# Kernel optimization log

Hardware: AMD Instinct MI355X
Metric: run time of the kernel (lower is better)

Reference implementation:

```python
import jax, jax.numpy as jnp
import numpy as np

N_NODES = 100000
N_EDGES = 1600000
IN_DIM = 256
HID = 128
OUT_DIM = 2
N_LAYERS = 4
BN_EPS = 1e-5


def setup_inputs() -> dict:
    key = jax.random.key(0)
    ks = jax.random.split(key, 10)
    s_in = 1.0 / np.sqrt(IN_DIM)
    s_h = 1.0 / np.sqrt(HID)
    return {
        "x": jax.random.normal(ks[0], (N_NODES, IN_DIM), dtype=jnp.float32),
        "edge_index": jax.random.randint(ks[1], (2, N_EDGES), 0, N_NODES, dtype=jnp.int32),
        "W_in": jax.random.normal(ks[2], (IN_DIM, HID), dtype=jnp.float32) * s_in,
        "b_in": jnp.zeros((HID,), dtype=jnp.float32),
        # SAGEConv per-layer weights: lin_l (aggregated neighbors), lin_r (self/root)
        "W_l": jax.random.normal(ks[3], (N_LAYERS, HID, HID), dtype=jnp.float32) * s_h,
        "b_l": jnp.zeros((N_LAYERS, HID), dtype=jnp.float32),
        "W_r": jax.random.normal(ks[4], (N_LAYERS, HID, HID), dtype=jnp.float32) * s_h,
        "b_r": jnp.zeros((N_LAYERS, HID), dtype=jnp.float32),
        # BatchNorm (eval mode) params/buffers
        "bn_gamma": jnp.ones((N_LAYERS, HID), dtype=jnp.float32),
        "bn_beta": jnp.zeros((N_LAYERS, HID), dtype=jnp.float32),
        "bn_mean": jax.random.normal(ks[5], (N_LAYERS, HID), dtype=jnp.float32) * 0.01,
        "bn_var": jnp.ones((N_LAYERS, HID), dtype=jnp.float32),
        "W_cls": jax.random.normal(ks[6], (HID, OUT_DIM), dtype=jnp.float32) * s_h,
        "b_cls": jnp.zeros((OUT_DIM,), dtype=jnp.float32),
    }


def _sage_mean(h, src, dst, n):
    # gather source-node features along edges, scatter-mean at targets
    msg = h[src]  # [E, HID] -- the large irregular gather
    agg = jax.ops.segment_sum(msg, dst, num_segments=n)  # [N, HID]
    cnt = jax.ops.segment_sum(jnp.ones((src.shape[0],), h.dtype), dst, num_segments=n)
    return agg / jnp.maximum(cnt, 1.0)[:, None]


def reference(x, edge_index, W_in, b_in, W_l, b_l, W_r, b_r,
              bn_gamma, bn_beta, bn_mean, bn_var, W_cls, b_cls):
    n = x.shape[0]
    src, dst = edge_index[0], edge_index[1]
    h = jax.nn.relu(x @ W_in + b_in)  # dropout is identity at eval
    for i in range(N_LAYERS):
        h_in = h
        mean = _sage_mean(h, src, dst, n)
        h = mean @ W_l[i] + b_l[i] + h @ W_r[i] + b_r[i]
        # BatchNorm1d in eval mode (running stats)
        h = bn_gamma[i] * (h - bn_mean[i]) * jax.lax.rsqrt(bn_var[i] + BN_EPS) + bn_beta[i]
        h = jax.nn.relu(h)
        h = h + h_in
    return jax.nn.log_softmax(h @ W_cls + b_cls, axis=1)
```

## Files before the change

### kernel.cpp

```cpp
#include <hip/hip_runtime.h>

typedef unsigned int uint;
typedef unsigned short ushort;
typedef __attribute__((ext_vector_type(8))) short short8v;
typedef __attribute__((ext_vector_type(4))) float f32x4;

#define IN_DIM 256
#define HID 128
#define BN_EPS 1e-5f

__device__ __forceinline__ float bf2f(ushort u) { return __uint_as_float(((uint)u) << 16); }
__device__ __forceinline__ ushort f2bf(float f) {
    uint u = __float_as_uint(f);
    return (ushort)((u + 0x7fffu + ((u >> 16) & 1u)) >> 16);
}
__device__ __forceinline__ uint cvt_pk_bf16(float a, float b) {
    uint r;
    asm("v_cvt_pk_bf16_f32 %0, %1, %2" : "=v"(r) : "v"(a), "v"(b));
    return r;
}
__device__ __forceinline__ void gload_lds16(const void* g, void* l) {
    __builtin_amdgcn_global_load_lds(
        (const __attribute__((address_space(1))) uint*)g,
        (__attribute__((address_space(3))) uint*)l, 16, 0, 0);
}


__global__ __launch_bounds__(256) void hist_kernel(const int* __restrict__ ei,
                                                   int* __restrict__ histG,
                                                   int E, int chunk) {
    __shared__ int hcnt[256];
    int t = threadIdx.x;
    hcnt[t] = 0;
    __syncthreads();
    int e0 = blockIdx.x * chunk;
    int e1 = min(E, e0 + chunk);
    for (int e = e0 + t; e < e1; e += 256)
        atomicAdd(&hcnt[__builtin_nontemporal_load(ei + E + e) >> 9], 1);
    __syncthreads();
    histG[blockIdx.x * 256 + t] = hcnt[t];
}

__global__ __launch_bounds__(256) void basescan_kernel(const int* __restrict__ histG,
                                                       int* __restrict__ baseG,
                                                       int* __restrict__ bucketStart,
                                                       int nchunk, int nbuck, int E) {
    __shared__ int sA[256], sB[256];
    int t = threadIdx.x;
    int tot = 0;
    for (int c = 0; c < nchunk; c++) tot += histG[c * 256 + t];
    sA[t] = tot;
    __syncthreads();
    int* src = sA; int* dst = sB;
    for (int off = 1; off < 256; off <<= 1) {
        int v = src[t];
        if (t >= off) v += src[t - off];
        dst[t] = v;
        __syncthreads();
        int* tmp = src; src = dst; dst = tmp;
    }
    int excl = src[t] - tot;
    if (t < nbuck) bucketStart[t] = excl;
    if (t == 0) bucketStart[nbuck] = E;
    int running = excl;
    for (int c = 0; c < nchunk; c++) {
        baseG[c * 256 + t] = running;
        running += histG[c * 256 + t];
    }
}

__global__ __launch_bounds__(256) void partition_kernel(const int* __restrict__ ei,
                                                        const int* __restrict__ baseG,
                                                        uint2* __restrict__ ebuck,
                                                        int E, int chunk) {
    __shared__ int cur[256];
    int t = threadIdx.x;
    cur[t] = baseG[blockIdx.x * 256 + t];
    __syncthreads();
    int e0 = blockIdx.x * chunk;
    int e1 = min(E, e0 + chunk);
    for (int e = e0 + t; e < e1; e += 256) {
        int d = __builtin_nontemporal_load(ei + E + e);
        int s = __builtin_nontemporal_load(ei + e);
        int pos = atomicAdd(&cur[d >> 9], 1);
        ebuck[pos] = make_uint2((uint)s, (uint)d);
    }
}

__global__ __launch_bounds__(256) void bucket_build(const uint2* __restrict__ ebuck,
                                                    const int* __restrict__ bucketStart,
                                                    int* __restrict__ row_ptr,
                                                    int* __restrict__ esrc,
                                                    int n, int nbuck) {
    __shared__ int deg[512];
    __shared__ int sA[512], sB[512];
    __shared__ int cur[512];
    __shared__ int img[16384];
    int b = blockIdx.x;
    int t = threadIdx.x;
    int lo = b << 9;
    int hi = min(n, lo + 512);
    int nn = hi - lo;
    int eStart = bucketStart[b];
    int eEnd = bucketStart[b + 1];
    int cnt = eEnd - eStart;
    for (int i = t; i < 512; i += 256) deg[i] = 0;
    __syncthreads();
    for (int e = eStart + t; e < eEnd; e += 256) {
        uint2 p = ebuck[e];
        atomicAdd(&deg[(int)p.y - lo], 1);
    }
    __syncthreads();
    for (int i = t; i < 512; i += 256) sA[i] = deg[i];
    __syncthreads();
    int* src = sA; int* dst = sB;
    for (int off = 1; off < 512; off <<= 1) {
        for (int i = t; i < 512; i += 256) {
            int v = src[i];
            if (i >= off) v += src[i - off];
            dst[i] = v;
        }
        __syncthreads();
        int* tmp = src; src = dst; dst = tmp;
    }
    for (int i = t; i < 512; i += 256) cur[i] = src[i] - deg[i];
    __syncthreads();
    for (int i = t; i < nn; i += 256) row_ptr[lo + i] = eStart + cur[i];
    if (b == nbuck - 1 && t == 0) row_ptr[n] = eEnd;
    __syncthreads();
    if (cnt <= 16384) {
        for (int e = eStart + t; e < eEnd; e += 256) {
            uint2 p = ebuck[e];
            int pos = atomicAdd(&cur[(int)p.y - lo], 1);
            img[pos] = (int)p.x;
        }
        __syncthreads();
        for (int i = t; i < cnt; i += 256) esrc[eStart + i] = img[i];
    } else {
        for (int e = eStart + t; e < eEnd; e += 256) {
            uint2 p = ebuck[e];
            int pos = atomicAdd(&cur[(int)p.y - lo], 1);
            esrc[eStart + pos] = (int)p.x;
        }
    }
}


__global__ __launch_bounds__(256) void pack_win(const float* __restrict__ W, ushort* __restrict__ Wt) {
    int idx = blockIdx.x * 256 + threadIdx.x;
    int k = idx >> 7, c = idx & 127;
    Wt[c * IN_DIM + k] = f2bf(W[idx]);
}

__global__ __launch_bounds__(256) void pack_wcat(const float* __restrict__ Wl,
                                                 const float* __restrict__ Wr,
                                                 ushort* __restrict__ Wt) {
    int idx = blockIdx.x * 256 + threadIdx.x;
    int layer = idx >> 15;
    int rem = idx & 32767;
    int k = rem >> 7, c = rem & 127;
    float v = (k < HID) ? Wl[layer * HID * HID + k * HID + c]
                        : Wr[layer * HID * HID + (k - HID) * HID + c];
    Wt[layer * (HID * 256) + c * 256 + k] = f2bf(v);
}


__global__ __launch_bounds__(256) void sage_mean_bf16(const ushort* __restrict__ h,
                                                      const int* __restrict__ row_ptr,
                                                      const int* __restrict__ esrc,
                                                      ushort* __restrict__ meanb, int n) {
    int node = blockIdx.x * 4 + (threadIdx.x >> 6);
    if (node >= n) return;
    int lane = threadIdx.x & 63;
    int start = row_ptr[node];
    int end = row_ptr[node + 1];
    float ax = 0.f, ay = 0.f;
    int j = start;
    for (; j + 15 < end; j += 16) {
        uint v[16];
        #pragma unroll
        for (int q = 0; q < 16; q++)
            v[q] = *(const uint*)(h + (size_t)esrc[j + q] * HID + lane * 2);
        #pragma unroll
        for (int q = 0; q < 16; q++) {
            ax += bf2f((ushort)(v[q] & 0xffffu));
            ay += bf2f((ushort)(v[q] >> 16));
        }
    }
    for (; j + 7 < end; j += 8) {
        uint v[8];
        #pragma unroll
        for (int q = 0; q < 8; q++)
            v[q] = *(const uint*)(h + (size_t)esrc[j + q] * HID + lane * 2);
        #pragma unroll
        for (int q = 0; q < 8; q++) {
            ax += bf2f((ushort)(v[q] & 0xffffu));
            ay += bf2f((ushort)(v[q] >> 16));
        }
    }
    for (; j < end; ++j) {
        uint v0 = *(const uint*)(h + (size_t)esrc[j] * HID + lane * 2);
        ax += bf2f((ushort)(v0 & 0xffffu));
        ay += bf2f((ushort)(v0 >> 16));
    }
    int deg = end - start;
    float inv = 1.0f / (float)(deg > 1 ? deg : 1);
    uint o = (uint)f2bf(ax * inv) | (((uint)f2bf(ay * inv)) << 16);
    *(uint*)(meanb + (size_t)node * HID + lane * 2) = o;
}


__global__ __launch_bounds__(256) void input_gemm_mfma(const float* __restrict__ x,
                                                       const ushort* __restrict__ Wt,
                                                       const float* __restrict__ b,
                                                       ushort* __restrict__ hout, int n) {
    __shared__ float Axs[32 * IN_DIM];
    int t = threadIdx.x;
    int l = t & 63;
    int wv = t >> 6;
    int colbase = wv * 32;
    int lr = l & 15;
    int grp = l >> 4;
    int ko = grp * 8;

    short8v Bf[8][2];
    #pragma unroll
    for (int ks = 0; ks < 8; ks++) {
        #pragma unroll
        for (int nt = 0; nt < 2; nt++) {
            int c = colbase + nt * 16 + lr;
            Bf[ks][nt] = *(const short8v*)(Wt + (size_t)c * IN_DIM + ks * 32 + ko);
        }
    }
    float bias0 = b[colbase + lr];
    float bias1 = b[colbase + 16 + lr];

    int ntiles = (n + 31) >> 5;
    for (int tile = blockIdx.x; tile < ntiles; tile += gridDim.x) {
        int row0 = tile * 32;
        __syncthreads();
        {
            const char* xb = (const char*)(x + (size_t)row0 * IN_DIM);
            char* lb = (char*)Axs;
            #pragma unroll
            for (int i = 0; i < 8; i++) {
                int off = i * 4096 + t * 16;
                int src = off ^ (((off >> 10) & 7) << 4);
                gload_lds16(xb + src, lb + i * 4096 + wv * 1024);
            }
        }
        __syncthreads();
        f32x4 acc00 = {0.f,0.f,0.f,0.f}, acc01 = {0.f,0.f,0.f,0.f};
        f32x4 acc10 = {0.f,0.f,0.f,0.f}, acc11 = {0.f,0.f,0.f,0.f};
        #pragma unroll
        for (int m = 0; m < 2; m++) {
            int r = m * 16 + lr;
            int rswz = (r & 7) << 4;
            const char* rowp = (const char*)Axs + r * 1024;
            short8v Af[8];
            #pragma unroll
            for (int ks = 0; ks < 8; ks++) {
                int kb = (ko + ks * 32) * 4;
                float4 p = *(const float4*)(rowp + (kb ^ rswz));
                float4 q = *(const float4*)(rowp + ((kb + 16) ^ rswz));
                union { uint4 u; short8v s; } cv;
                cv.u.x = cvt_pk_bf16(p.x, p.y);
                cv.u.y = cvt_pk_bf16(p.z, p.w);
                cv.u.z = cvt_pk_bf16(q.x, q.y);
                cv.u.w = cvt_pk_bf16(q.z, q.w);
                Af[ks] = cv.s;
            }
            if (m == 0) {
                #pragma unroll
                for (int ks = 0; ks < 8; ks++) {
                    acc00 = __builtin_amdgcn_mfma_f32_16x16x32_bf16(Af[ks], Bf[ks][0], acc00, 0, 0, 0);
                    acc01 = __builtin_amdgcn_mfma_f32_16x16x32_bf16(Af[ks], Bf[ks][1], acc01, 0, 0, 0);
                }
            } else {
                #pragma unroll
                for (int ks = 0; ks < 8; ks++) {
                    acc10 = __builtin_amdgcn_mfma_f32_16x16x32_bf16(Af[ks], Bf[ks][0], acc10, 0, 0, 0);
                    acc11 = __builtin_amdgcn_mfma_f32_16x16x32_bf16(Af[ks], Bf[ks][1], acc11, 0, 0, 0);
                }
            }
        }
        #pragma unroll
        for (int m = 0; m < 2; m++) {
            int rbase = row0 + m * 16 + grp * 4;
            f32x4 a0 = m == 0 ? acc00 : acc10;
            f32x4 a1 = m == 0 ? acc01 : acc11;
            #pragma unroll
            for (int r = 0; r < 4; r++) {
                int rowd = rbase + r;
                if (rowd < n) {
                    float z0 = a0[r] + bias0; z0 = z0 > 0.f ? z0 : 0.f;
                    float z1 = a1[r] + bias1; z1 = z1 > 0.f ? z1 : 0.f;
                    hout[(size_t)rowd * HID + colbase + lr] = f2bf(z0);
                    hout[(size_t)rowd * HID + colbase + 16 + lr] = f2bf(z1);
                }
            }
        }
    }
}


__global__ __launch_bounds__(256) void sage_layer_mfma(const ushort* __restrict__ h,
                                                       const ushort* __restrict__ mh,
                                                       ushort* __restrict__ hout,
                                                       const ushort* __restrict__ Wt,
                                                       const float* __restrict__ bl,
                                                       const float* __restrict__ br,
                                                       const float* __restrict__ gamma,
                                                       const float* __restrict__ beta,
                                                       const float* __restrict__ bmean,
                                                       const float* __restrict__ bvar,
                                                       int n) {
    __shared__ ushort Ams[64 * HID];
    __shared__ ushort Ahs[64 * HID];
    int t = threadIdx.x;
    int l = t & 63;
    int wv = t >> 6;
    int colbase = wv * 32;
    int lr = l & 15;
    int grp = l >> 4;
    int ko = grp * 8;

    short8v Bf[8][2];
    #pragma unroll
    for (int ks = 0; ks < 8; ks++) {
        #pragma unroll
        for (int nt = 0; nt < 2; nt++) {
            int c = colbase + nt * 16 + lr;
            Bf[ks][nt] = *(const short8v*)(Wt + (size_t)c * 256 + ks * 32 + ko);
        }
    }
    int c0 = colbase + lr;
    int c1 = c0 + 16;
    float scale0 = gamma[c0] * rsqrtf(bvar[c0] + BN_EPS);
    float scale1 = gamma[c1] * rsqrtf(bvar[c1] + BN_EPS);
    float shift0 = beta[c0] + (bl[c0] + br[c0] - bmean[c0]) * scale0;
    float shift1 = beta[c1] + (bl[c1] + br[c1] - bmean[c1]) * scale1;

    int ntiles = (n + 63) >> 6;
    for (int tile = blockIdx.x; tile < ntiles; tile += gridDim.x) {
        int row0 = tile * 64;
        __syncthreads();
        {
            const char* mb = (const char*)(mh + (size_t)row0 * HID);
            const char* hb = (const char*)(h + (size_t)row0 * HID);
            char* lm = (char*)Ams;
            char* lh = (char*)Ahs;
            #pragma unroll
            for (int i = 0; i < 4; i++) {
                int off = i * 4096 + t * 16;
                int src = off ^ (((off >> 8) & 7) << 4);
                gload_lds16(mb + src, lm + i * 4096 + wv * 1024);
                gload_lds16(hb + src, lh + i * 4096 + wv * 1024);
            }
        }
        __syncthreads();
        #pragma unroll
        for (int m = 0; m < 4; m++) {
            int r = m * 16 + lr;
            int rswz = (r & 7) << 4;
            const char* mrow = (const char*)Ams + r * 256;
            const char* hrow = (const char*)Ahs + r * 256;
            short8v Af[8];
            #pragma unroll
            for (int ks = 0; ks < 4; ks++) {
                int kb = (ko + ks * 32) * 2;
                Af[ks] = *(const short8v*)(mrow + (kb ^ rswz));
            }
            #pragma unroll
            for (int ks = 4; ks < 8; ks++) {
                int kb = (ko + (ks - 4) * 32) * 2;
                Af[ks] = *(const short8v*)(hrow + (kb ^ rswz));
            }
            f32x4 acc0 = {0.f,0.f,0.f,0.f};
            f32x4 acc1 = {0.f,0.f,0.f,0.f};
            #pragma unroll
            for (int ks = 0; ks < 8; ks++) {
                acc0 = __builtin_amdgcn_mfma_f32_16x16x32_bf16(Af[ks], Bf[ks][0], acc0, 0, 0, 0);
                acc1 = __builtin_amdgcn_mfma_f32_16x16x32_bf16(Af[ks], Bf[ks][1], acc1, 0, 0, 0);
            }
            int rbase = m * 16 + grp * 4;
            #pragma unroll
            for (int r2 = 0; r2 < 4; r2++) {
                int rloc = rbase + r2;
                int rowd = row0 + rloc;
                if (rowd < n) {
                    int rs = (rloc & 7) << 4;
                    float res0 = bf2f(*(const ushort*)((const char*)Ahs + rloc * 256 + ((c0 * 2) ^ rs)));
                    float res1 = bf2f(*(const ushort*)((const char*)Ahs + rloc * 256 + ((c1 * 2) ^ rs)));
                    float z0 = acc0[r2] * scale0 + shift0; z0 = z0 > 0.f ? z0 : 0.f;
                    float z1 = acc1[r2] * scale1 + shift1; z1 = z1 > 0.f ? z1 : 0.f;
                    hout[(size_t)rowd * HID + c0] = f2bf(z0 + res0);
                    hout[(size_t)rowd * HID + c1] = f2bf(z1 + res1);
                }
            }
        }
    }
}


__global__ __launch_bounds__(256) void classifier_bf16(const ushort* __restrict__ h,
                                                       const float* __restrict__ Wc,
                                                       const float* __restrict__ bc,
                                                       float* __restrict__ outp, int n) {
    __shared__ float Wcs[HID * 2];
    int t = threadIdx.x;
    if (t < 64) *(float4*)&Wcs[t * 4] = *(const float4*)&Wc[t * 4];
    __syncthreads();
    int rowInBlk = t >> 4;
    int sub = t & 15;
    int row = blockIdx.x * 16 + rowInBlk;
    float l0 = 0.f, l1 = 0.f;
    if (row < n) {
        const ushort* hr = h + (size_t)row * HID + sub * 8;
        uint4 v = *(const uint4*)hr;
        float e0 = bf2f((ushort)(v.x & 0xffffu)), e1 = bf2f((ushort)(v.x >> 16));
        float e2 = bf2f((ushort)(v.y & 0xffffu)), e3 = bf2f((ushort)(v.y >> 16));
        float e4 = bf2f((ushort)(v.z & 0xffffu)), e5 = bf2f((ushort)(v.z >> 16));
        float e6 = bf2f((ushort)(v.w & 0xffffu)), e7 = bf2f((ushort)(v.w >> 16));
        int k0 = sub * 8;
        l0 += e0 * Wcs[(k0 + 0) * 2] + e1 * Wcs[(k0 + 1) * 2] + e2 * Wcs[(k0 + 2) * 2] + e3 * Wcs[(k0 + 3) * 2];
        l0 += e4 * Wcs[(k0 + 4) * 2] + e5 * Wcs[(k0 + 5) * 2] + e6 * Wcs[(k0 + 6) * 2] + e7 * Wcs[(k0 + 7) * 2];
        l1 += e0 * Wcs[(k0 + 0) * 2 + 1] + e1 * Wcs[(k0 + 1) * 2 + 1] + e2 * Wcs[(k0 + 2) * 2 + 1] + e3 * Wcs[(k0 + 3) * 2 + 1];
        l1 += e4 * Wcs[(k0 + 4) * 2 + 1] + e5 * Wcs[(k0 + 5) * 2 + 1] + e6 * Wcs[(k0 + 6) * 2 + 1] + e7 * Wcs[(k0 + 7) * 2 + 1];
    }
    #pragma unroll
    for (int off = 1; off < 16; off <<= 1) {
        l0 += __shfl_xor(l0, off);
        l1 += __shfl_xor(l1, off);
    }
    if (sub == 0 && row < n) {
        l0 += bc[0];
        l1 += bc[1];
        float m = fmaxf(l0, l1);
        float lse = m + logf(expf(l0 - m) + expf(l1 - m));
        outp[(size_t)row * 2 + 0] = l0 - lse;
        outp[(size_t)row * 2 + 1] = l1 - lse;
    }
}


extern "C" void kernel_launch(void* const* d_in, const int* in_sizes, int n_in,
                              void* d_out, int out_size, void* d_ws, size_t ws_size,
                              hipStream_t stream) {
    const float* x     = (const float*)d_in[0];
    const int*   ei    = (const int*)d_in[1];
    const float* W_in  = (const float*)d_in[2];
    const float* b_in  = (const float*)d_in[3];
    const float* W_l   = (const float*)d_in[4];
    const float* b_l   = (const float*)d_in[5];
    const float* W_r   = (const float*)d_in[6];
    const float* b_r   = (const float*)d_in[7];
    const float* bn_g  = (const float*)d_in[8];
    const float* bn_b  = (const float*)d_in[9];
    const float* bn_m  = (const float*)d_in[10];
    const float* bn_v  = (const float*)d_in[11];
    const float* W_cls = (const float*)d_in[12];
    const float* b_cls = (const float*)d_in[13];
    float* outp = (float*)d_out;

    const int N = in_sizes[0] / IN_DIM;
    const int E = in_sizes[1] / 2;

    char* w = (char*)d_ws;
    const size_t HB = (size_t)N * HID * sizeof(ushort);
    ushort* hA     = (ushort*)(w);
    ushort* hB     = (ushort*)(w + HB);
    ushort* meanb  = (ushort*)(w + 2 * HB);
    ushort* Wt_in  = (ushort*)(w + 3 * HB);
    ushort* WcatT  = (ushort*)(w + 3 * HB + 65536);
    size_t off = 3 * HB + 65536 + 262144;
    int* row_ptr = (int*)(w + off);  off += ((size_t)(N + 1) * 4 + 255) & ~(size_t)255;
    int* esrc    = (int*)(w + off);  off += (size_t)E * 4;
    uint2* ebuck = (uint2*)(w + off); off += (size_t)E * 8;
    int* histG   = (int*)(w + off);  off += 256 * 256 * 4;
    int* baseG   = (int*)(w + off);  off += 256 * 256 * 4;
    int* bucketStart = (int*)(w + off); off += 4096;

    const int nbuck = (N + 511) >> 9;
    const int nchunk = 256;
    const int chunk = (E + nchunk - 1) / nchunk;

    pack_win<<<128, 256, 0, stream>>>(W_in, Wt_in);
    pack_wcat<<<512, 256, 0, stream>>>(W_l, W_r, WcatT);

    hist_kernel<<<nchunk, 256, 0, stream>>>(ei, histG, E, chunk);
    basescan_kernel<<<1, 256, 0, stream>>>(histG, baseG, bucketStart, nchunk, nbuck, E);
    partition_kernel<<<nchunk, 256, 0, stream>>>(ei, baseG, ebuck, E, chunk);
    bucket_build<<<nbuck, 256, 0, stream>>>(ebuck, bucketStart, row_ptr, esrc, N, nbuck);

    input_gemm_mfma<<<(N + 31) / 32, 256, 0, stream>>>(x, Wt_in, b_in, hA, N);

    ushort* hcur = hA;
    ushort* hoth = hB;
    for (int i = 0; i < 4; i++) {
        sage_mean_bf16<<<(N + 3) / 4, 256, 0, stream>>>(hcur, row_ptr, esrc, meanb, N);
        sage_layer_mfma<<<(N + 63) / 64, 256, 0, stream>>>(hcur, meanb, hoth,
                                                  WcatT + (size_t)i * HID * 256,
                                                  b_l + i * HID, b_r + i * HID,
                                                  bn_g + i * HID, bn_b + i * HID,
                                                  bn_m + i * HID, bn_v + i * HID, N);
        ushort* tmp = hcur; hcur = hoth; hoth = tmp;
    }

    classifier_bf16<<<(N + 15) / 16, 256, 0, stream>>>(hcur, W_cls, b_cls, outp, N);
}
```

Before: 529.5 us.

## Fuse neighbor mean aggregation into SAGE layer GEMM kernel via LDS

The separate mean-aggregation kernel is removed. Each wave of the layer kernel now gathers and averages neighbor features for 16 rows of its 64-row tile, writing the bf16 means straight into swizzled LDS before the MFMA step. This drops the write and re-read of the mean buffer and one launch per layer. The cost is that the irregular gather now runs in a kernel with large LDS and register use, so it may get less occupancy and latency hiding than the standalone kernel had, and the gather and GEMM phases are serialized within each block.

```diff
diff --git a/kernel.cpp b/kernel.cpp
--- a/kernel.cpp
+++ b/kernel.cpp
@@ -165,51 +165,6 @@
 }
 
 
-__global__ __launch_bounds__(256) void sage_mean_bf16(const ushort* __restrict__ h,
-                                                      const int* __restrict__ row_ptr,
-                                                      const int* __restrict__ esrc,
-                                                      ushort* __restrict__ meanb, int n) {
-    int node = blockIdx.x * 4 + (threadIdx.x >> 6);
-    if (node >= n) return;
-    int lane = threadIdx.x & 63;
-    int start = row_ptr[node];
-    int end = row_ptr[node + 1];
-    float ax = 0.f, ay = 0.f;
-    int j = start;
-    for (; j + 15 < end; j += 16) {
-        uint v[16];
-        #pragma unroll
-        for (int q = 0; q < 16; q++)
-            v[q] = *(const uint*)(h + (size_t)esrc[j + q] * HID + lane * 2);
-        #pragma unroll
-        for (int q = 0; q < 16; q++) {
-            ax += bf2f((ushort)(v[q] & 0xffffu));
-            ay += bf2f((ushort)(v[q] >> 16));
-        }
-    }
-    for (; j + 7 < end; j += 8) {
-        uint v[8];
-        #pragma unroll
-        for (int q = 0; q < 8; q++)
-            v[q] = *(const uint*)(h + (size_t)esrc[j + q] * HID + lane * 2);
-        #pragma unroll
-        for (int q = 0; q < 8; q++) {
-            ax += bf2f((ushort)(v[q] & 0xffffu));
-            ay += bf2f((ushort)(v[q] >> 16));
-        }
-    }
-    for (; j < end; ++j) {
-        uint v0 = *(const uint*)(h + (size_t)esrc[j] * HID + lane * 2);
-        ax += bf2f((ushort)(v0 & 0xffffu));
-        ay += bf2f((ushort)(v0 >> 16));
-    }
-    int deg = end - start;
-    float inv = 1.0f / (float)(deg > 1 ? deg : 1);
-    uint o = (uint)f2bf(ax * inv) | (((uint)f2bf(ay * inv)) << 16);
-    *(uint*)(meanb + (size_t)node * HID + lane * 2) = o;
-}
-
-
 __global__ __launch_bounds__(256) void input_gemm_mfma(const float* __restrict__ x,
                                                        const ushort* __restrict__ Wt,
                                                        const float* __restrict__ b,
@@ -304,17 +259,18 @@
 }
 
 
-__global__ __launch_bounds__(256) void sage_layer_mfma(const ushort* __restrict__ h,
-                                                       const ushort* __restrict__ mh,
-                                                       ushort* __restrict__ hout,
-                                                       const ushort* __restrict__ Wt,
-                                                       const float* __restrict__ bl,
-                                                       const float* __restrict__ br,
-                                                       const float* __restrict__ gamma,
-                                                       const float* __restrict__ beta,
-                                                       const float* __restrict__ bmean,
-                                                       const float* __restrict__ bvar,
-                                                       int n) {
+__global__ __launch_bounds__(256) void sage_fused(const ushort* __restrict__ h,
+                                                  ushort* __restrict__ hout,
+                                                  const int* __restrict__ row_ptr,
+                                                  const int* __restrict__ esrc,
+                                                  const ushort* __restrict__ Wt,
+                                                  const float* __restrict__ bl,
+                                                  const float* __restrict__ br,
+                                                  const float* __restrict__ gamma,
+                                                  const float* __restrict__ beta,
+                                                  const float* __restrict__ bmean,
+                                                  const float* __restrict__ bvar,
+                                                  int n) {
     __shared__ ushort Ams[64 * HID];
     __shared__ ushort Ahs[64 * HID];
     int t = threadIdx.x;
@@ -346,17 +302,56 @@
         int row0 = tile * 64;
         __syncthreads();
         {
-            const char* mb = (const char*)(mh + (size_t)row0 * HID);
             const char* hb = (const char*)(h + (size_t)row0 * HID);
-            char* lm = (char*)Ams;
             char* lh = (char*)Ahs;
             #pragma unroll
             for (int i = 0; i < 4; i++) {
                 int off = i * 4096 + t * 16;
                 int src = off ^ (((off >> 8) & 7) << 4);
-                gload_lds16(mb + src, lm + i * 4096 + wv * 1024);
                 gload_lds16(hb + src, lh + i * 4096 + wv * 1024);
             }
+        }
+        for (int i = 0; i < 16; i++) {
+            int r = wv * 16 + i;
+            int node = row0 + r;
+            float ax = 0.f, ay = 0.f;
+            if (node < n) {
+                int start = row_ptr[node];
+                int end = row_ptr[node + 1];
+                int j = start;
+                for (; j + 15 < end; j += 16) {
+                    uint v[16];
+                    #pragma unroll
+                    for (int q = 0; q < 16; q++)
+                        v[q] = *(const uint*)(h + (size_t)esrc[j + q] * HID + l * 2);
+                    #pragma unroll
+                    for (int q = 0; q < 16; q++) {
+                        ax += bf2f((ushort)(v[q] & 0xffffu));
+                        ay += bf2f((ushort)(v[q] >> 16));
+                    }
+                }
+                for (; j + 7 < end; j += 8) {
+                    uint v[8];
+                    #pragma unroll
+                    for (int q = 0; q < 8; q++)
+                        v[q] = *(const uint*)(h + (size_t)esrc[j + q] * HID + l * 2);
+                    #pragma unroll
+                    for (int q = 0; q < 8; q++) {
+                        ax += bf2f((ushort)(v[q] & 0xffffu));
+                        ay += bf2f((ushort)(v[q] >> 16));
+                    }
+                }
+                for (; j < end; ++j) {
+                    uint v0 = *(const uint*)(h + (size_t)esrc[j] * HID + l * 2);
+                    ax += bf2f((ushort)(v0 & 0xffffu));
+                    ay += bf2f((ushort)(v0 >> 16));
+                }
+                int deg = end - start;
+                float inv = 1.0f / (float)(deg > 1 ? deg : 1);
+                ax *= inv; ay *= inv;
+            }
+            uint o = (uint)f2bf(ax) | (((uint)f2bf(ay)) << 16);
+            *(uint*)((char*)Ams + r * 256 + ((l * 4) ^ ((r & 7) << 4))) = o;
         }
         __syncthreads();
         #pragma unroll
@@ -480,6 +475,7 @@
     int* histG   = (int*)(w + off);  off += 256 * 256 * 4;
     int* baseG   = (int*)(w + off);  off += 256 * 256 * 4;
     int* bucketStart = (int*)(w + off); off += 4096;
+    (void)meanb;
 
     const int nbuck = (N + 511) >> 9;
     const int nchunk = 256;
@@ -498,12 +494,11 @@
     ushort* hcur = hA;
     ushort* hoth = hB;
     for (int i = 0; i < 4; i++) {
-        sage_mean_bf16<<<(N + 3) / 4, 256, 0, stream>>>(hcur, row_ptr, esrc, meanb, N);
-        sage_layer_mfma<<<(N + 63) / 64, 256, 0, stream>>>(hcur, meanb, hoth,
-                                                  WcatT + (size_t)i * HID * 256,
-                                                  b_l + i * HID, b_r + i * HID,
-                                                  bn_g + i * HID, bn_b + i * HID,
-                                                  bn_m + i * HID, bn_v + i * HID, N);
+        sage_fused<<<(N + 63) / 64, 256, 0, stream>>>(hcur, hoth, row_ptr, esrc,
+                                                      WcatT + (size_t)i * HID * 256,
+                                                      b_l + i * HID, b_r + i * HID,
+                                                      bn_g + i * HID, bn_b + i * HID,
+                                                      bn_m + i * HID, bn_v + i * HID, N);
         ushort* tmp = hcur; hcur = hoth; hoth = tmp;
     }
 
```

Result: slower. 1.009 ms (+90.5%).
